# Optimization experiments

Hardware: AMD Instinct MI355X
Metric: run time of the kernel (lower is better)

## Reference

```python
import jax, jax.numpy as jnp
import numpy as np
import math

B, LD, LQ, D = 8, 1024, 1024, 256
ITER = 1

def setup_inputs() -> dict:
    key = jax.random.key(0)
    ks = jax.random.split(key, 24)
    s = 1.0 / math.sqrt(D)
    w = lambda k: (jax.random.normal(k, (D, D), dtype=jnp.float32) * s)
    inp = {
        'd_node': jax.random.normal(ks[0], (B, LD, D), dtype=jnp.float32),
        'q_node': jax.random.normal(ks[1], (B, LQ, D), dtype=jnp.float32),
        'W_dq_query': w(ks[2]), 'W_dk_key': w(ks[3]),
        'W_qq_query': w(ks[4]), 'W_qk_key': w(ks[5]),
        'W_dq_fc': w(ks[6]), 'W_qd_fc': w(ks[7]),
        'W_self': w(ks[8]), 'b_self': jnp.zeros((D,), dtype=jnp.float32),
        'W_dd_l': w(ks[9]), 'W_qq_l': w(ks[10]), 'W_dq_l': w(ks[11]), 'W_qd_l': w(ks[12]),
        'W_dd_r': w(ks[13]), 'W_qq_r': w(ks[14]), 'W_dq_r': w(ks[15]), 'W_qd_r': w(ks[16]),
        'd_node_mask': jax.random.randint(ks[17], (B, LD), 0, 2).astype(jnp.int32),
        'q_node_mask': jax.random.randint(ks[18], (B, LQ), 0, 2).astype(jnp.int32),
        'ner_mask': jax.random.randint(ks[19], (B, LD + LQ, LD + LQ), 0, 2).astype(jnp.int32),
        'graph': jax.random.randint(ks[20], (B, LD + LQ, LD + LQ), 0, 2).astype(jnp.int32),
    }
    return inp

def _lin(x, W):
    # torch Linear: y = x @ W.T
    return jnp.einsum('bld,ed->ble', x, W)

def gcn_forward(d_node, q_node, W_dq_query, W_dk_key, W_qq_query, W_qk_key,
                W_dq_fc, W_qd_fc, W_self, b_self,
                W_dd_l, W_qq_l, W_dq_l, W_qd_l,
                W_dd_r, W_qq_r, W_dq_r, W_qd_r,
                d_node_mask, q_node_mask, ner_mask, graph):
    Ld = d_node.shape[1]; Lq = q_node.shape[1]
    dk = d_node.shape[-1]
    eye_d = jnp.eye(Ld, dtype=graph.dtype)
    eye_q = jnp.eye(Lq, dtype=graph.dtype)
    # relation masks [B,L,L] (int)
    d_mask = d_node_mask[:, None, :] * d_node_mask[:, :, None] * ner_mask[:, :Ld, :Ld]
    dd_graph = d_mask * (1 - eye_d)[None]
    g_dd = graph[:, :Ld, :Ld]
    dd_l = dd_graph * g_dd; dd_r = dd_graph * (1 - g_dd)
    q_mask = q_node_mask[:, None, :] * q_node_mask[:, :, None] * ner_mask[:, Ld:, Ld:]
    qq_graph = q_mask * (1 - eye_q)[None]
    g_qq = graph[:, Ld:, Ld:]
    qq_l = qq_graph * g_qq; qq_r = qq_graph * (1 - g_qq)
    dq_graph = d_node_mask[:, :, None] * q_node_mask[:, None, :] * ner_mask[:, :Ld, Ld:]
    g_dq = graph[:, :Ld, Ld:]
    dq_l = dq_graph * g_dq; dq_r = dq_graph * (1 - g_dq)
    qd_graph = q_node_mask[:, :, None] * d_node_mask[:, None, :] * ner_mask[:, Ld:, :Ld]
    g_qd = graph[:, Ld:, :Ld]
    qd_l = qd_graph * g_qd; qd_r = qd_graph * (1 - g_qd)
    # neighbor counts, replace 0 -> 1
    d_nb = (dd_l.sum(-1) + dd_r.sum(-1) + dq_l.sum(-1) + dq_r.sum(-1)).astype(jnp.float32)
    d_nb = jnp.where(d_nb >= 1, d_nb, 1.0)
    q_nb = (qq_l.sum(-1) + qq_r.sum(-1) + qd_l.sum(-1) + qd_r.sum(-1)).astype(jnp.float32)
    q_nb = jnp.where(q_nb >= 1, q_nb, 1.0)
    NEG = -1.0e9
    scale = 1.0 / math.sqrt(dk)
    f = jnp.float32
    dd_lf, dd_rf = dd_l.astype(f), dd_r.astype(f)
    qq_lf, qq_rf = qq_l.astype(f), qq_r.astype(f)
    dq_lf, dq_rf = dq_l.astype(f), dq_r.astype(f)
    qd_lf, qd_rf = qd_l.astype(f), qd_r.astype(f)
    for _ in range(ITER):
        d_scores = jnp.einsum('bid,bjd->bij', _lin(d_node, W_dq_query), _lin(d_node, W_dk_key)) * scale
        d_attn = jax.nn.softmax(jnp.where(d_mask == 0, NEG, d_scores), axis=-1)
        q_scores = jnp.einsum('bid,bjd->bij', _lin(q_node, W_qq_query), _lin(q_node, W_qk_key)) * scale
        q_attn = jax.nn.softmax(jnp.where(q_mask == 0, NEG, q_scores), axis=-1)
        dq_scores = jnp.einsum('bid,bjd->bij', d_node, _lin(q_node, W_dq_fc))
        dq_attn = jax.nn.softmax(jnp.where(dq_graph == 0, NEG, dq_scores), axis=-1)
        qd_scores = jnp.einsum('bid,bjd->bij', q_node, _lin(d_node, W_qd_fc))
        qd_attn = jax.nn.softmax(jnp.where(qd_graph == 0, NEG, qd_scores), axis=-1)
        self_d = _lin(d_node, W_self) + b_self
        self_q = _lin(q_node, W_self) + b_self
        # left aggregation (graph_left entries are 0/1 -> masking == multiply)
        dd_il = jnp.einsum('bij,bjd->bid', d_attn * dd_lf, _lin(d_node, W_dd_l))
        qd_il = jnp.einsum('bij,bjd->bid', qd_attn * qd_lf, _lin(d_node, W_qd_l))
        qq_il = jnp.einsum('bij,bjd->bid', q_attn * qq_lf, _lin(q_node, W_qq_l))
        dq_il = jnp.einsum('bij,bjd->bid', dq_attn * dq_lf, _lin(q_node, W_dq_l))
        # right aggregation
        dd_ir = jnp.einsum('bij,bjd->bid', d_attn * dd_rf, _lin(d_node, W_dd_r))
        qd_ir = jnp.einsum('bij,bjd->bid', qd_attn * qd_rf, _lin(d_node, W_qd_r))
        qq_ir = jnp.einsum('bij,bjd->bid', q_attn * qq_rf, _lin(q_node, W_qq_r))
        dq_ir = jnp.einsum('bij,bjd->bid', dq_attn * dq_rf, _lin(q_node, W_dq_r))
        agg_d = (dd_il + dd_ir + dq_il + dq_ir) / d_nb[:, :, None]
        agg_q = (qq_il + qq_ir + qd_il + qd_ir) / q_nb[:, :, None]
        d_node = jax.nn.relu(self_d + agg_d)
        q_node = jax.nn.relu(self_q + agg_q)
    return (d_node, q_node)

def reference(d_node, q_node, W_dq_query, W_dk_key, W_qq_query, W_qk_key,
              W_dq_fc, W_qd_fc, W_self, b_self,
              W_dd_l, W_qq_l, W_dq_l, W_qd_l,
              W_dd_r, W_qq_r, W_dq_r, W_qd_r,
              d_node_mask, q_node_mask, ner_mask, graph):
    return gcn_forward(d_node, q_node, W_dq_query, W_dk_key, W_qq_query, W_qk_key,
                       W_dq_fc, W_qd_fc, W_self, b_self,
                       W_dd_l, W_qq_l, W_dq_l, W_qd_l,
                       W_dd_r, W_qq_r, W_dq_r, W_qd_r,
                       d_node_mask, q_node_mask, ner_mask, graph)
```

## Files before the change

kernel.cpp:

```cpp
#include <hip/hip_runtime.h>
#include <stdint.h>

typedef __attribute__((ext_vector_type(8))) short s16x8;
typedef __attribute__((ext_vector_type(4))) float f32x4;
typedef unsigned short u16;

#define DEV static __device__ __forceinline__

DEV f32x4 mfma16(s16x8 a, s16x8 b, f32x4 c) {
    return __builtin_amdgcn_mfma_f32_16x16x32_bf16(a, b, c, 0, 0, 0);
}

DEV void gld16(const void* g, void* l) {
    __builtin_amdgcn_global_load_lds(
        (const __attribute__((address_space(1))) void*)g,
        (__attribute__((address_space(3))) void*)l, 16, 0, 0);
}

DEV u16 f2bf(float x) {
    union { float f; unsigned u; } v; v.f = x;
    unsigned r = v.u + 0x7FFFu + ((v.u >> 16) & 1u);
    return (u16)(r >> 16);
}
DEV float bf2f(u16 h) { return __uint_as_float(((unsigned)h) << 16); }

struct WPtrs { const float* p[16]; };

__global__ void k_conv_w(WPtrs wp, u16* wd, u16* wq) {
    int t = blockIdx.x * 256 + threadIdx.x;
    int mat = t >> 14;
    int e = (t & 16383) << 2;
    const float* s = wp.p[mat] + e;
    u16* d = (mat < 8 ? wd + mat * 65536 : wq + (mat - 8) * 65536) + e;
    float4 v = *(const float4*)s;
    d[0] = f2bf(v.x); d[1] = f2bf(v.y); d[2] = f2bf(v.z); d[3] = f2bf(v.w);
}

__global__ void k_conv_x(const float* dn, const float* qn, u16* xd, u16* xq) {
    int t = blockIdx.x * 256 + threadIdx.x;
    int h = t >> 19;
    int e = (t & 524287) << 2;
    const float* s = (h ? qn : dn) + e;
    u16* d = (h ? xq : xd) + e;
    float4 v = *(const float4*)s;
    d[0] = f2bf(v.x); d[1] = f2bf(v.y); d[2] = f2bf(v.z); d[3] = f2bf(v.w);
}

__global__ __launch_bounds__(256, 1) void k_proj(const u16* xd, const u16* xq,
        const u16* wdm, const u16* wqm, u16* tokd, u16* tokq, u16* vtd, u16* vtq) {
    __shared__ __align__(16) char smem[16384];
    char* As = smem; char* Bs = smem + 8192;
    const int lane = threadIdx.x & 63, wid = threadIdx.x >> 6;
    const int z = blockIdx.z, grp = z >> 3, w = z & 7;
    const u16* X = grp ? xq : xd;
    const u16* W = (grp ? wqm : wdm) + w * 65536;
    const int m0 = blockIdx.x * 128, n0 = blockIdx.y * 128;
    const int wr = wid >> 1, wc = wid & 1;
    const int rl = lane & 15, g = lane >> 4;
    const f32x4 fz = {0.f, 0.f, 0.f, 0.f};
    f32x4 acc[4][4];
#pragma unroll
    for (int i = 0; i < 4; ++i)
#pragma unroll
        for (int j = 0; j < 4; ++j) acc[i][j] = fz;

    for (int kt = 0; kt < 8; ++kt) {
#pragma unroll
        for (int t = 0; t < 2; ++t) {
            int iid = wid * 2 + t;
            int ldso = iid * 1024 + lane * 16;
            int row = ldso >> 6, inrow = ldso & 63;
            int src = inrow ^ ((row & 3) << 4);
            gld16((const char*)X + ((size_t)(m0 + row) * 512 + kt * 64 + src), As + iid * 1024);
            gld16((const char*)W + ((size_t)(n0 + row) * 512 + kt * 64 + src), Bs + iid * 1024);
        }
        __syncthreads();
        s16x8 av[4], bv[4];
#pragma unroll
        for (int rf = 0; rf < 4; ++rf) {
            int row = wr * 64 + rf * 16 + rl;
            av[rf] = *(const s16x8*)(As + row * 64 + ((g * 16) ^ ((row & 3) << 4)));
        }
#pragma unroll
        for (int cf = 0; cf < 4; ++cf) {
            int row = wc * 64 + cf * 16 + rl;
            bv[cf] = *(const s16x8*)(Bs + row * 64 + ((g * 16) ^ ((row & 3) << 4)));
        }
#pragma unroll
        for (int rf = 0; rf < 4; ++rf)
#pragma unroll
            for (int cf = 0; cf < 4; ++cf)
                acc[rf][cf] = mfma16(av[rf], bv[cf], acc[rf][cf]);
        __syncthreads();
    }
    if (w < 4) {
        u16* out = (grp ? tokq : tokd) + (size_t)w * 2097152;
#pragma unroll
        for (int rf = 0; rf < 4; ++rf)
#pragma unroll
            for (int cf = 0; cf < 4; ++cf) {
                int n = n0 + wc * 64 + cf * 16 + rl;
                int m = m0 + wr * 64 + rf * 16 + g * 4;
#pragma unroll
                for (int r = 0; r < 4; ++r)
                    out[(size_t)(m + r) * 256 + n] = f2bf(acc[rf][cf][r]);
            }
    } else {
        u16* out = (grp ? vtq : vtd) + (size_t)(w - 4) * 2097152;
#pragma unroll
        for (int rf = 0; rf < 4; ++rf)
#pragma unroll
            for (int cf = 0; cf < 4; ++cf) {
                int n = n0 + wc * 64 + cf * 16 + rl;
                int m = m0 + wr * 64 + rf * 16 + g * 4;
                int b = m >> 10, tok = m & 1023;
                unsigned lo = (unsigned)f2bf(acc[rf][cf][0]) | ((unsigned)f2bf(acc[rf][cf][1]) << 16);
                unsigned hi = (unsigned)f2bf(acc[rf][cf][2]) | ((unsigned)f2bf(acc[rf][cf][3]) << 16);
                uint2 u; u.x = lo; u.y = hi;
                *(uint2*)(out + ((size_t)(b * 256 + n)) * 1024 + tok) = u;
            }
    }
}

struct PhaseCfg {
    const void* Q; const u16* K; const u16* Vl; const u16* Vr;
    const int* rm; const int* cm;
    int roff, coff; float scale;
    float* io; float* nbOut; const float* nbIn; const u16* selfTok;
};

template<bool FINAL>
__global__ __launch_bounds__(256, 1) void k_attn(PhaseCfg c0, PhaseCfg c1,
        const int* ner, const int* graph, const float* bias) {
    const PhaseCfg c = blockIdx.z ? c1 : c0;
    const int b = blockIdx.y;
    const int i0 = blockIdx.x * 64;
    const int lane = threadIdx.x & 63, wid = threadIdx.x >> 6;
    const int rl = lane & 15, g = lane >> 4;

    __shared__ __align__(16) char smem[60160];
    char* Ks  = smem;
    char* Vls = smem + 16384;
    char* Vrs = smem + 32768;
    u16* Pls = (u16*)(smem + 49152);
    u16* Prs = (u16*)(smem + 54272);
    float* rsS = (float*)(smem + 59392);
    float* dnS = (float*)(smem + 59648);
    float* nbS = (float*)(smem + 59904);

    s16x8 qf[8];
    {
        int qrow = i0 + wid * 16 + rl;
        if (FINAL) {
            const float* Qp = (const float*)c.Q + (size_t)(b * 1024 + qrow) * 256 + g * 8;
#pragma unroll
            for (int kf = 0; kf < 8; ++kf) {
                float4 x = *(const float4*)(Qp + kf * 32);
                float4 y = *(const float4*)(Qp + kf * 32 + 4);
                s16x8 t;
                t[0]=(short)f2bf(x.x); t[1]=(short)f2bf(x.y); t[2]=(short)f2bf(x.z); t[3]=(short)f2bf(x.w);
                t[4]=(short)f2bf(y.x); t[5]=(short)f2bf(y.y); t[6]=(short)f2bf(y.z); t[7]=(short)f2bf(y.w);
                qf[kf] = t;
            }
        } else {
            const u16* Qb = (const u16*)c.Q + (size_t)(b * 1024 + qrow) * 256 + g * 8;
#pragma unroll
            for (int kf = 0; kf < 8; ++kf) qf[kf] = *(const s16x8*)(Qb + kf * 32);
        }
    }
    int rmv[4];
#pragma unroll
    for (int r = 0; r < 4; ++r)
        rmv[r] = c.rm[b * 1024 + i0 + wid * 16 + g * 4 + r] != 0;

    const f32x4 fz = {0.f,0.f,0.f,0.f};
    f32x4 accl[4][4], accr[4][4];
#pragma unroll
    for (int i = 0; i < 4; ++i)
#pragma unroll
        for (int j = 0; j < 4; ++j) { accl[i][j] = fz; accr[i][j] = fz; }
    float mrow[4] = {-1e30f,-1e30f,-1e30f,-1e30f};
    float dden[4] = {0.f,0.f,0.f,0.f};
    float nbc[4]  = {0.f,0.f,0.f,0.f};

    const char* Kg  = (const char*)c.K  + (size_t)b * 524288;
    const char* Vlg = (const char*)c.Vl + (size_t)b * 524288;
    const char* Vrg = (const char*)c.Vr + (size_t)b * 524288;

    for (int jt = 0; jt < 32; ++jt) {
        const int j0 = jt * 32;
        __syncthreads();
#pragma unroll
        for (int t = 0; t < 4; ++t) {
            int iid = wid * 4 + t;
            int ldso = iid * 1024 + lane * 16;
            int row = ldso >> 9, inrow = ldso & 511;
            int src = inrow ^ ((row & 7) << 4);
            gld16(Kg + ((size_t)(j0 + row) * 512 + src), Ks + iid * 1024);
        }
#pragma unroll
        for (int t = 0; t < 4; ++t) {
            int iid = wid * 4 + t;
            int ldso = iid * 1024 + lane * 16;
            int cc = ldso >> 6, in = ldso & 63;
            int src = in ^ ((cc & 3) << 4);
            gld16(Vlg + ((size_t)cc * 2048 + (size_t)j0 * 2 + src), Vls + iid * 1024);
            gld16(Vrg + ((size_t)cc * 2048 + (size_t)j0 * 2 + src), Vrs + iid * 1024);
        }
        __syncthreads();

        f32x4 s0 = fz, s1 = fz;
#pragma unroll
        for (int kk = 0; kk < 8; ++kk) {
            int jr0 = rl, jr1 = 16 + rl;
            s16x8 b0 = *(const s16x8*)(Ks + jr0 * 512 + ((kk * 64 + g * 16) ^ ((jr0 & 7) << 4)));
            s16x8 b1 = *(const s16x8*)(Ks + jr1 * 512 + ((kk * 64 + g * 16) ^ ((jr1 & 7) << 4)));
            s0 = mfma16(qf[kk], b0, s0);
            s1 = mfma16(qf[kk], b1, s1);
        }

        const int iqb = i0 + wid * 16 + g * 4;
        const int jq0 = j0 + rl, jq1 = j0 + 16 + rl;
        const int cm0 = c.cm[b * 1024 + jq0] != 0;
        const int cm1 = c.cm[b * 1024 + jq1] != 0;
        float sv0[4], sv1[4];
        int l0[4], l1[4], r0m[4], r1m[4];
#pragma unroll
        for (int r = 0; r < 4; ++r) {
            int iq = iqb + r;
            size_t mb = ((size_t)(b * 2048 + c.roff + iq)) * 2048 + c.coff;
            int n0v = ner[mb + jq0] != 0, n1v = ner[mb + jq1] != 0;
            int g0v = graph[mb + jq0] != 0, g1v = graph[mb + jq1] != 0;
            int v0 = rmv[r] & cm0 & n0v;
            int v1 = rmv[r] & cm1 & n1v;
            int e0 = FINAL ? v0 : (v0 & (int)(iq != jq0));
            int e1 = FINAL ? v1 : (v1 & (int)(iq != jq1));
            sv0[r] = v0 ? s0[r] * c.scale : -1e30f;
            sv1[r] = v1 ? s1[r] * c.scale : -1e30f;
            l0[r] = e0 & g0v;  r0m[r] = e0 & (g0v ^ 1);
            l1[r] = e1 & g1v;  r1m[r] = e1 & (g1v ^ 1);
            nbc[r] += (float)(e0 + e1);
        }
        float rsv[4];
#pragma unroll
        for (int r = 0; r < 4; ++r) {
            float t = fmaxf(sv0[r], sv1[r]);
            t = fmaxf(t, __shfl_xor(t, 1));
            t = fmaxf(t, __shfl_xor(t, 2));
            t = fmaxf(t, __shfl_xor(t, 4));
            t = fmaxf(t, __shfl_xor(t, 8));
            float mn = fmaxf(mrow[r], t);
            rsv[r] = __expf(mrow[r] - mn);
            mrow[r] = mn;
            float e0 = __expf(sv0[r] - mn);
            float e1 = __expf(sv1[r] - mn);
            dden[r] = dden[r] * rsv[r] + e0 + e1;
            int prow = wid * 16 + g * 4 + r;
            Pls[prow * 40 + rl]      = l0[r]  ? f2bf(e0) : (u16)0;
            Pls[prow * 40 + 16 + rl] = l1[r]  ? f2bf(e1) : (u16)0;
            Prs[prow * 40 + rl]      = r0m[r] ? f2bf(e0) : (u16)0;
            Prs[prow * 40 + 16 + rl] = r1m[r] ? f2bf(e1) : (u16)0;
        }
        if (rl == 0) {
            f32x4 rv = {rsv[0], rsv[1], rsv[2], rsv[3]};
            *(f32x4*)(rsS + wid * 16 + g * 4) = rv;
        }
        __syncthreads();

        f32x4 rs4[4];
#pragma unroll
        for (int rf = 0; rf < 4; ++rf) rs4[rf] = *(const f32x4*)(rsS + rf * 16 + g * 4);
#pragma unroll
        for (int rf = 0; rf < 4; ++rf)
#pragma unroll
            for (int cf = 0; cf < 4; ++cf) { accl[rf][cf] *= rs4[rf]; accr[rf][cf] *= rs4[rf]; }
        s16x8 pa[4], pb[4], va[4], vb[4];
#pragma unroll
        for (int rf = 0; rf < 4; ++rf) {
            pa[rf] = *(const s16x8*)((char*)Pls + (rf * 16 + rl) * 80 + g * 16);
            pb[rf] = *(const s16x8*)((char*)Prs + (rf * 16 + rl) * 80 + g * 16);
        }
#pragma unroll
        for (int cf = 0; cf < 4; ++cf) {
            int cc = wid * 64 + cf * 16 + rl;
            int off = (g * 16) ^ ((cc & 3) << 4);
            va[cf] = *(const s16x8*)(Vls + cc * 64 + off);
            vb[cf] = *(const s16x8*)(Vrs + cc * 64 + off);
        }
#pragma unroll
        for (int rf = 0; rf < 4; ++rf)
#pragma unroll
            for (int cf = 0; cf < 4; ++cf) {
                accl[rf][cf] = mfma16(pa[rf], va[cf], accl[rf][cf]);
                accr[rf][cf] = mfma16(pb[rf], vb[cf], accr[rf][cf]);
            }
    }

#pragma unroll
    for (int r = 0; r < 4; ++r) {
        float d = dden[r];
        d += __shfl_xor(d, 1); d += __shfl_xor(d, 2); d += __shfl_xor(d, 4); d += __shfl_xor(d, 8);
        dden[r] = d;
        float nn = nbc[r];
        nn += __shfl_xor(nn, 1); nn += __shfl_xor(nn, 2); nn += __shfl_xor(nn, 4); nn += __shfl_xor(nn, 8);
        nbc[r] = nn;
    }
    if (rl == 0) {
        f32x4 dv = {dden[0], dden[1], dden[2], dden[3]};
        *(f32x4*)(dnS + wid * 16 + g * 4) = dv;
        int idx = b * 1024 + i0 + wid * 16 + g * 4;
        if (!FINAL) {
            f32x4 nv = {nbc[0], nbc[1], nbc[2], nbc[3]};
            *(f32x4*)(c.nbOut + idx) = nv;
        } else {
            f32x4 nv = {nbc[0] + c.nbIn[idx], nbc[1] + c.nbIn[idx + 1],
                        nbc[2] + c.nbIn[idx + 2], nbc[3] + c.nbIn[idx + 3]};
            *(f32x4*)(nbS + wid * 16 + g * 4) = nv;
        }
    }
    __syncthreads();

    float bcol[4];
    if (FINAL) {
#pragma unroll
        for (int cf = 0; cf < 4; ++cf) bcol[cf] = bias[wid * 64 + cf * 16 + rl];
    }
#pragma unroll
    for (int rf = 0; rf < 4; ++rf) {
        f32x4 dv = *(const f32x4*)(dnS + rf * 16 + g * 4);
        f32x4 nbv = fz;
        if (FINAL) nbv = *(const f32x4*)(nbS + rf * 16 + g * 4);
#pragma unroll
        for (int cf = 0; cf < 4; ++cf) {
            int col = wid * 64 + cf * 16 + rl;
#pragma unroll
            for (int r = 0; r < 4; ++r) {
                int row = i0 + rf * 16 + g * 4 + r;
                size_t oi = (size_t)(b * 1024 + row) * 256 + col;
                float inv = dv[r] > 0.f ? 1.f / dv[r] : 0.f;
                float v = (accl[rf][cf][r] + accr[rf][cf][r]) * inv;
                if (!FINAL) {
                    c.io[oi] = v;
                } else {
                    float nb = fmaxf(nbv[r], 1.f);
                    float agg = (c.io[oi] + v) / nb;
                    float sf = bf2f(c.selfTok[oi]) + bcol[cf];
                    c.io[oi] = fmaxf(sf + agg, 0.f);
                }
            }
        }
    }
}

extern "C" void kernel_launch(void* const* d_in, const int* in_sizes, int n_in,
                              void* d_out, int out_size, void* d_ws, size_t ws_size,
                              hipStream_t stream) {
    (void)in_sizes; (void)n_in; (void)out_size; (void)ws_size;
    const float* d_node = (const float*)d_in[0];
    const float* q_node = (const float*)d_in[1];
    const float* b_self = (const float*)d_in[9];
    const int* dm = (const int*)d_in[18];
    const int* qm = (const int*)d_in[19];
    const int* ner = (const int*)d_in[20];
    const int* graph = (const int*)d_in[21];

    char* ws = (char*)d_ws;
    const size_t MB = 1024 * 1024;
    u16* xd   = (u16*)(ws + 0 * MB);
    u16* xq   = (u16*)(ws + 4 * MB);
    u16* wdm  = (u16*)(ws + 8 * MB);
    u16* wqm  = (u16*)(ws + 9 * MB);
    u16* tokd = (u16*)(ws + 10 * MB);
    u16* tokq = (u16*)(ws + 26 * MB);
    u16* vtd  = (u16*)(ws + 42 * MB);
    u16* vtq  = (u16*)(ws + 58 * MB);
    float* nbdd = (float*)(ws + 74 * MB);
    float* nbqq = (float*)(ws + 74 * MB + 32768);

    float* outd = (float*)d_out;
    float* outq = outd + 2097152;

    WPtrs wp;
    wp.p[0]  = (const float*)d_in[2];
    wp.p[1]  = (const float*)d_in[3];
    wp.p[2]  = (const float*)d_in[7];
    wp.p[3]  = (const float*)d_in[8];
    wp.p[4]  = (const float*)d_in[10];
    wp.p[5]  = (const float*)d_in[14];
    wp.p[6]  = (const float*)d_in[13];
    wp.p[7]  = (const float*)d_in[17];
    wp.p[8]  = (const float*)d_in[4];
    wp.p[9]  = (const float*)d_in[5];
    wp.p[10] = (const float*)d_in[6];
    wp.p[11] = (const float*)d_in[8];
    wp.p[12] = (const float*)d_in[11];
    wp.p[13] = (const float*)d_in[15];
    wp.p[14] = (const float*)d_in[12];
    wp.p[15] = (const float*)d_in[16];

    k_conv_w<<<1024, 256, 0, stream>>>(wp, wdm, wqm);
    k_conv_x<<<4096, 256, 0, stream>>>(d_node, q_node, xd, xq);
    k_proj<<<dim3(64, 2, 16), 256, 0, stream>>>(xd, xq, wdm, wqm, tokd, tokq, vtd, vtq);

    const size_t M2 = 2097152;
    PhaseCfg dd = { tokd, tokd + M2, vtd, vtd + M2, dm, dm, 0, 0, 0.0625f,
                    outd, nbdd, nullptr, nullptr };
    PhaseCfg qq = { tokq, tokq + M2, vtq, vtq + M2, qm, qm, 1024, 1024, 0.0625f,
                    outq, nbqq, nullptr, nullptr };
    k_attn<false><<<dim3(16, 8, 2), 256, 0, stream>>>(dd, qq, ner, graph, b_self);

    PhaseCfg dq = { d_node, tokq + 2 * M2, vtq + 2 * M2, vtq + 3 * M2, dm, qm, 0, 1024, 1.0f,
                    outd, nullptr, nbdd, tokd + 3 * M2 };
    PhaseCfg qd = { q_node, tokd + 2 * M2, vtd + 2 * M2, vtd + 3 * M2, qm, dm, 1024, 0, 1.0f,
                    outq, nullptr, nbqq, tokq + 3 * M2 };
    k_attn<true><<<dim3(16, 8, 2), 256, 0, stream>>>(dq, qd, ner, graph, b_self);
}
```

Baseline: 313.9 us.

## Double-buffer K/V tiles in LDS and prefetch mask loads one tile ahead

Switches the attention kernel to dynamic shared memory holding two K/Vl/Vr buffers. The next tile is issued via global_load_lds while the current one is computed, using manual vmcnt waits and scheduler barriers in place of __syncthreads. The ner/graph/column-mask loads for the next tile are also issued early into registers. This is meant to hide global latency in a grid of only 256 single-block-per-CU workgroups, at the cost of roughly doubled LDS use, extra registers, and fragile hand-counted waitcnt values.

```diff
diff --git a/kernel.cpp b/kernel.cpp
--- a/kernel.cpp
+++ b/kernel.cpp
@@ -23,6 +23,9 @@
     return (u16)(r >> 16);
 }
 DEV float bf2f(u16 h) { return __uint_as_float(((unsigned)h) << 16); }
+
+#define SBAR() do { __builtin_amdgcn_sched_barrier(0); __builtin_amdgcn_s_barrier(); __builtin_amdgcn_sched_barrier(0); } while (0)
+#define LGKM0() asm volatile("s_waitcnt lgkmcnt(0)" ::: "memory")
 
 struct WPtrs { const float* p[16]; };
 
@@ -138,15 +141,12 @@
     const int lane = threadIdx.x & 63, wid = threadIdx.x >> 6;
     const int rl = lane & 15, g = lane >> 4;
 
-    __shared__ __align__(16) char smem[60160];
-    char* Ks  = smem;
-    char* Vls = smem + 16384;
-    char* Vrs = smem + 32768;
-    u16* Pls = (u16*)(smem + 49152);
-    u16* Prs = (u16*)(smem + 54272);
-    float* rsS = (float*)(smem + 59392);
-    float* dnS = (float*)(smem + 59648);
-    float* nbS = (float*)(smem + 59904);
+    extern __shared__ char smem[];
+    u16* Pls = (u16*)(smem + 98304);
+    u16* Prs = (u16*)(smem + 103424);
+    float* rsS = (float*)(smem + 108544);
+    float* dnS = (float*)(smem + 108800);
+    float* nbS = (float*)(smem + 109056);
 
     s16x8 qf[8];
     {
@@ -168,10 +168,16 @@
             for (int kf = 0; kf < 8; ++kf) qf[kf] = *(const s16x8*)(Qb + kf * 32);
         }
     }
+    const int iqb = i0 + wid * 16 + g * 4;
     int rmv[4];
 #pragma unroll
     for (int r = 0; r < 4; ++r)
-        rmv[r] = c.rm[b * 1024 + i0 + wid * 16 + g * 4 + r] != 0;
+        rmv[r] = c.rm[b * 1024 + iqb + r] != 0;
+
+    const size_t mb0 = ((size_t)(b * 2048 + c.roff + iqb)) * 2048 + c.coff;
+    const int* nrb = ner + mb0;
+    const int* grb = graph + mb0;
+    const int* cmp = c.cm + b * 1024;
 
     const f32x4 fz = {0.f,0.f,0.f,0.f};
     f32x4 accl[4][4], accr[4][4];
@@ -187,16 +193,17 @@
     const char* Vlg = (const char*)c.Vl + (size_t)b * 524288;
     const char* Vrg = (const char*)c.Vr + (size_t)b * 524288;
 
-    for (int jt = 0; jt < 32; ++jt) {
-        const int j0 = jt * 32;
-        __syncthreads();
+    auto STAGE = [&](int j0, int sel) {
+        char* Kd  = smem + sel * 16384;
+        char* Vld = smem + 32768 + sel * 16384;
+        char* Vrd = smem + 65536 + sel * 16384;
 #pragma unroll
         for (int t = 0; t < 4; ++t) {
             int iid = wid * 4 + t;
             int ldso = iid * 1024 + lane * 16;
             int row = ldso >> 9, inrow = ldso & 511;
             int src = inrow ^ ((row & 7) << 4);
-            gld16(Kg + ((size_t)(j0 + row) * 512 + src), Ks + iid * 1024);
+            gld16(Kg + ((size_t)(j0 + row) * 512 + src), Kd + iid * 1024);
         }
 #pragma unroll
         for (int t = 0; t < 4; ++t) {
@@ -204,10 +211,42 @@
             int ldso = iid * 1024 + lane * 16;
             int cc = ldso >> 6, in = ldso & 63;
             int src = in ^ ((cc & 3) << 4);
-            gld16(Vlg + ((size_t)cc * 2048 + (size_t)j0 * 2 + src), Vls + iid * 1024);
-            gld16(Vrg + ((size_t)cc * 2048 + (size_t)j0 * 2 + src), Vrs + iid * 1024);
-        }
-        __syncthreads();
+            gld16(Vlg + ((size_t)cc * 2048 + (size_t)j0 * 2 + src), Vld + iid * 1024);
+            gld16(Vrg + ((size_t)cc * 2048 + (size_t)j0 * 2 + src), Vrd + iid * 1024);
+        }
+    };
+
+    int mn0[4], mn1[4], mg0[4], mg1[4], mc0, mc1;
+    auto MLOAD = [&](int j0) {
+        int jq0 = j0 + rl, jq1 = j0 + 16 + rl;
+#pragma unroll
+        for (int r = 0; r < 4; ++r) {
+            mn0[r] = nrb[r * 2048 + jq0];
+            mn1[r] = nrb[r * 2048 + jq1];
+            mg0[r] = grb[r * 2048 + jq0];
+            mg1[r] = grb[r * 2048 + jq1];
+        }
+        mc0 = cmp[jq0]; mc1 = cmp[jq1];
+    };
+
+    STAGE(0, 0);
+    MLOAD(0);
+
+#pragma unroll 1
+    for (int jt = 0; jt < 32; ++jt) {
+        const int sel = jt & 1;
+        const int j0 = jt * 32;
+        if (jt < 31) {
+            STAGE(j0 + 32, sel ^ 1);
+            asm volatile("s_waitcnt vmcnt(30)" ::: "memory");
+        } else {
+            asm volatile("s_waitcnt vmcnt(18)" ::: "memory");
+        }
+        SBAR();
+
+        const char* Ks  = smem + sel * 16384;
+        const char* Vls = smem + 32768 + sel * 16384;
+        const char* Vrs = smem + 65536 + sel * 16384;
 
         f32x4 s0 = fz, s1 = fz;
 #pragma unroll
@@ -219,18 +258,15 @@
             s1 = mfma16(qf[kk], b1, s1);
         }
 
-        const int iqb = i0 + wid * 16 + g * 4;
         const int jq0 = j0 + rl, jq1 = j0 + 16 + rl;
-        const int cm0 = c.cm[b * 1024 + jq0] != 0;
-        const int cm1 = c.cm[b * 1024 + jq1] != 0;
+        const int cm0 = mc0 != 0, cm1 = mc1 != 0;
         float sv0[4], sv1[4];
         int l0[4], l1[4], r0m[4], r1m[4];
 #pragma unroll
         for (int r = 0; r < 4; ++r) {
             int iq = iqb + r;
-            size_t mb = ((size_t)(b * 2048 + c.roff + iq)) * 2048 + c.coff;
-            int n0v = ner[mb + jq0] != 0, n1v = ner[mb + jq1] != 0;
-            int g0v = graph[mb + jq0] != 0, g1v = graph[mb + jq1] != 0;
+            int n0v = mn0[r] != 0, n1v = mn1[r] != 0;
+            int g0v = mg0[r] != 0, g1v = mg1[r] != 0;
             int v0 = rmv[r] & cm0 & n0v;
             int v1 = rmv[r] & cm1 & n1v;
             int e0 = FINAL ? v0 : (v0 & (int)(iq != jq0));
@@ -265,7 +301,10 @@
             f32x4 rv = {rsv[0], rsv[1], rsv[2], rsv[3]};
             *(f32x4*)(rsS + wid * 16 + g * 4) = rv;
         }
-        __syncthreads();
+        LGKM0();
+        SBAR();
+
+        if (jt < 31) MLOAD(j0 + 32);
 
         f32x4 rs4[4];
 #pragma unroll
@@ -294,6 +333,8 @@
                 accl[rf][cf] = mfma16(pa[rf], va[cf], accl[rf][cf]);
                 accr[rf][cf] = mfma16(pb[rf], vb[cf], accr[rf][cf]);
             }
+        LGKM0();
+        SBAR();
     }
 
 #pragma unroll
@@ -398,6 +439,12 @@
     wp.p[14] = (const float*)d_in[12];
     wp.p[15] = (const float*)d_in[16];
 
+    const int SMEM = 109312;
+    (void)hipFuncSetAttribute((const void*)k_attn<false>,
+        hipFuncAttributeMaxDynamicSharedMemorySize, SMEM);
+    (void)hipFuncSetAttribute((const void*)k_attn<true>,
+        hipFuncAttributeMaxDynamicSharedMemorySize, SMEM);
+
     k_conv_w<<<1024, 256, 0, stream>>>(wp, wdm, wqm);
     k_conv_x<<<4096, 256, 0, stream>>>(d_node, q_node, xd, xq);
     k_proj<<<dim3(64, 2, 16), 256, 0, stream>>>(xd, xq, wdm, wqm, tokd, tokq, vtd, vtq);
@@ -407,11 +454,11 @@
                     outd, nbdd, nullptr, nullptr };
     PhaseCfg qq = { tokq, tokq + M2, vtq, vtq + M2, qm, qm, 1024, 1024, 0.0625f,
                     outq, nbqq, nullptr, nullptr };
-    k_attn<false><<<dim3(16, 8, 2), 256, 0, stream>>>(dd, qq, ner, graph, b_self);
+    k_attn<false><<<dim3(16, 8, 2), 256, SMEM, stream>>>(dd, qq, ner, graph, b_self);
 
     PhaseCfg dq = { d_node, tokq + 2 * M2, vtq + 2 * M2, vtq + 3 * M2, dm, qm, 0, 1024, 1.0f,
                     outd, nullptr, nbdd, tokd + 3 * M2 };
     PhaseCfg qd = { q_node, tokd + 2 * M2, vtd + 2 * M2, vtd + 3 * M2, qm, dm, 1024, 0, 1.0f,
                     outq, nullptr, nbqq, tokq + 3 * M2 };
-    k_attn<true><<<dim3(16, 8, 2), 256, 0, stream>>>(dq, qd, ner, graph, b_self);
-}
+    k_attn<true><<<dim3(16, 8, 2), 256, SMEM, stream>>>(dq, qd, ner, graph, b_self);
+}
```

Result: slower. 323.2 us (+3.0%).
